# Kernel tuning notes

Hardware: AMD Instinct MI355X
Metric: run time of the kernel (lower is better)

The kernel has to match this reference:

```python
import jax, jax.numpy as jnp
import numpy as np

B, T, D = 2, 2048, 2048
H, HKV, HD = 32, 8, 64
THETA = 3.0
EPS = 1e-6
SCALE = HD ** -0.5


def _rms(x, w):
    # x: [..., HD]
    return x * jax.lax.rsqrt(jnp.mean(x * x, axis=-1, keepdims=True) + EPS) * w


def _rope(x):
    # x: [B, h, T, HD]; interleaved-pair rotation, matching RotaryEmbedding
    hd = x.shape[-1]
    inv_freq = 1.0 / (THETA ** (jnp.arange(0, hd, 2, dtype=jnp.float32) / hd))  # [hd/2]
    t = jnp.arange(x.shape[-2], dtype=jnp.float32)
    f = t[:, None] * inv_freq[None, :]  # [T, hd/2]
    c, s = jnp.cos(f), jnp.sin(f)
    x1, x2 = x[..., 0::2], x[..., 1::2]
    return jnp.stack([x1 * c - x2 * s, x1 * s + x2 * c], axis=-1).reshape(x.shape)


def setup_inputs() -> dict:
    key = jax.random.key(0)
    ks = jax.random.split(key, 6)
    x = jax.random.normal(ks[0], (B, T, D), dtype=jnp.float32)
    w_scale = 1.0 / np.sqrt(D)
    Wq = jax.random.normal(ks[1], (H * HD, D), dtype=jnp.float32) * w_scale
    Wk = jax.random.normal(ks[2], (HKV * HD, D), dtype=jnp.float32) * w_scale
    Wv = jax.random.normal(ks[3], (HKV * HD, D), dtype=jnp.float32) * w_scale
    Wo = jax.random.normal(ks[4], (D, H * HD), dtype=jnp.float32) * (1.0 / np.sqrt(H * HD))
    q_norm_w = jnp.ones((HD,), dtype=jnp.float32)
    k_norm_w = jnp.ones((HD,), dtype=jnp.float32)
    causal = jnp.tril(jnp.ones((T, T), dtype=bool))
    mask = jnp.where(causal, 0.0, -1e9).astype(jnp.float32)[None, None]  # [1,1,T,T]
    return dict(x=x, Wq=Wq, Wk=Wk, Wv=Wv, Wo=Wo, q_norm_w=q_norm_w, k_norm_w=k_norm_w, mask=mask)


def reference(x, Wq, Wk, Wv, Wo, q_norm_w, k_norm_w, mask):
    b, t, _ = x.shape
    q = (x @ Wq.T).reshape(b, t, H, HD).transpose(0, 2, 1, 3)      # [B,H,T,HD]
    k = (x @ Wk.T).reshape(b, t, HKV, HD).transpose(0, 2, 1, 3)    # [B,HKV,T,HD]
    v = (x @ Wv.T).reshape(b, t, HKV, HD).transpose(0, 2, 1, 3)
    q = _rms(q, q_norm_w)
    k = _rms(k, k_norm_w)
    q = _rope(q)
    k = _rope(k)
    rep = H // HKV
    k = jnp.repeat(k, rep, axis=1)  # GQA expansion -> [B,H,T,HD]
    v = jnp.repeat(v, rep, axis=1)
    scores = jnp.einsum('bhqd,bhkd->bhqk', q, k) * SCALE + mask
    attn = jax.nn.softmax(scores, axis=-1)
    out = jnp.einsum('bhqk,bhkd->bhqd', attn, v)
    out = out.transpose(0, 2, 1, 3).reshape(b, t, H * HD)
    return out @ Wo.T
```

## Files before the change

kernel.cpp:

```cpp
#include <hip/hip_runtime.h>
#include <hip/hip_bf16.h>
#include <stdint.h>

#define B_ 2
#define T_ 2048
#define D_ 2048
#define H_ 32
#define HKV_ 8
#define HD_ 64
#define SCALE_ 0.125f

typedef float floatx4 __attribute__((ext_vector_type(4)));
typedef __bf16 bf16x8 __attribute__((ext_vector_type(8)));
typedef __bf16 bf16x4 __attribute__((ext_vector_type(4)));
typedef short short4v __attribute__((ext_vector_type(4)));

__device__ inline floatx4 mfma16(bf16x8 a, bf16x8 b, floatx4 c) {
  return __builtin_amdgcn_mfma_f32_16x16x32_bf16(a, b, c, 0, 0, 0);
}

__device__ inline floatx4 mfma16k16(bf16x4 a, bf16x4 b, floatx4 c) {
#if __has_builtin(__builtin_amdgcn_mfma_f32_16x16x16_bf16)
  return __builtin_amdgcn_mfma_f32_16x16x16_bf16(a, b, c, 0, 0, 0);
#else
  return __builtin_amdgcn_mfma_f32_16x16x16bf16_1k(
      __builtin_bit_cast(short4v, a), __builtin_bit_cast(short4v, b), c, 0, 0, 0);
#endif
}

__device__ inline uint16_t f2bf(float f) {
  union { float f; uint32_t u; } x; x.f = f;
  uint32_t r = x.u + 0x7fffu + ((x.u >> 16) & 1u);
  return (uint16_t)(r >> 16);
}

__device__ inline uint32_t f2bf_pk(float a, float b) {
#if __has_builtin(__builtin_amdgcn_cvt_pk_bf16_f32)
  auto pk = __builtin_amdgcn_cvt_pk_bf16_f32(a, b);
  return __builtin_bit_cast(uint32_t, pk);
#else
  return (uint32_t)f2bf(a) | ((uint32_t)f2bf(b) << 16);
#endif
}

__device__ inline uint32_t pack_p(float a, float b) {
#if __has_builtin(__builtin_amdgcn_cvt_pk_bf16_f32)
  auto pk = __builtin_amdgcn_cvt_pk_bf16_f32(a, b);
  return __builtin_bit_cast(uint32_t, pk);
#else
  return __builtin_amdgcn_perm(__builtin_bit_cast(uint32_t, b),
                               __builtin_bit_cast(uint32_t, a), 0x07060302u);
#endif
}

__device__ inline float fast_exp2(float x) {
#if __has_builtin(__builtin_amdgcn_exp2f)
  return __builtin_amdgcn_exp2f(x);
#else
  return __expf(x * 0.69314718056f);
#endif
}

#if __has_builtin(__builtin_amdgcn_global_load_lds)
#define HAVE_ASYNC_LDS 1
typedef const __attribute__((address_space(1))) uint32_t* gas1_u32;
typedef __attribute__((address_space(3))) uint32_t* las3_u32;
__device__ inline void g2lds16(const uint16_t* g, uint16_t* l) {
  __builtin_amdgcn_global_load_lds((gas1_u32)(const void*)g, (las3_u32)(void*)l, 16, 0, 0);
}
#endif

__global__ __launch_bounds__(256) void cvt_all(
    const float* __restrict__ x, const float* __restrict__ wq,
    const float* __restrict__ wk, const float* __restrict__ wv,
    const float* __restrict__ wo,
    uint16_t* __restrict__ xb, uint16_t* __restrict__ wqb,
    uint16_t* __restrict__ wkb, uint16_t* __restrict__ wvb,
    uint16_t* __restrict__ wob) {
  int i = blockIdx.x * 256 + threadIdx.x;
  const float* src; uint16_t* dst; int off;
  if (i < 2097152)      { src = x;  dst = xb;  off = i; }
  else if (i < 3145728) { src = wq; dst = wqb; off = i - 2097152; }
  else if (i < 3407872) { src = wk; dst = wkb; off = i - 3145728; }
  else if (i < 3670016) { src = wv; dst = wvb; off = i - 3407872; }
  else                  { src = wo; dst = wob; off = i - 3670016; }
  float4 v = ((const float4*)src)[off];
  uint64_t packed = (uint64_t)f2bf_pk(v.x, v.y) | ((uint64_t)f2bf_pk(v.z, v.w) << 32);
  ((uint64_t*)dst)[off] = packed;
}

#define BM 128
#define BN 128

__device__ inline bf16x8 frag32(const uint16_t* lds, int row, int quad) {
  int pcg = quad ^ ((row >> 1) & 3);
  return *(const bf16x8*)&lds[row * 32 + pcg * 8];
}


#define GEMM_PROLOGUE()                                                    \
  const int srow = tid >> 2;                                               \
  const int scg = (tid & 3) ^ ((tid >> 3) & 3);                            \
  const uint16_t* gA0 = Abase + (size_t)srow * D_ + scg * 8;               \
  const uint16_t* gA1 = gA0 + (size_t)64 * D_;                             \
  const uint16_t* gB0 = Bbase + (size_t)srow * D_ + scg * 8;               \
  const uint16_t* gB1 = gB0 + (size_t)64 * D_;                             \
  uint16_t* lA[2] = {As + tid * 8, As + 4096 + tid * 8};                   \
  uint16_t* lB[2] = {Bs + tid * 8, Bs + 4096 + tid * 8};

#ifdef HAVE_ASYNC_LDS
#define GEMM_STAGE(buf, k)                                                 \
  { g2lds16(gA0 + (k), lA[buf]); g2lds16(gA1 + (k), lA[buf] + 2048);       \
    g2lds16(gB0 + (k), lB[buf]); g2lds16(gB1 + (k), lB[buf] + 2048); }
#else
#define GEMM_STAGE(buf, k)                                                 \
  { *(uint4*)lA[buf] = *(const uint4*)(gA0 + (k));                         \
    *(uint4*)(lA[buf] + 2048) = *(const uint4*)(gA1 + (k));                \
    *(uint4*)lB[buf] = *(const uint4*)(gB0 + (k));                         \
    *(uint4*)(lB[buf] + 2048) = *(const uint4*)(gB1 + (k)); }
#endif

#define GEMM_KLOOP()                                                       \
  GEMM_PROLOGUE()                                                          \
  GEMM_STAGE(0, 0)                                                         \
  int cur = 0;                                                             \
  for (int k0 = 0; k0 < D_; k0 += 32) {                                    \
    __syncthreads();                                                       \
    if (k0 + 32 < D_) { GEMM_STAGE(cur ^ 1, k0 + 32) }                     \
    const uint16_t* Ac = As + cur * 4096;                                  \
    const uint16_t* Bc = Bs + cur * 4096;                                  \
    bf16x8 af[4], bfr[4];                                                  \
    _Pragma("unroll")                                                      \
    for (int i = 0; i < 4; i++) af[i] = frag32(Ac, wm + i * 16 + r16, quad); \
    _Pragma("unroll")                                                      \
    for (int j = 0; j < 4; j++) bfr[j] = frag32(Bc, wn + j * 16 + r16, quad); \
    _Pragma("unroll")                                                      \
    for (int i = 0; i < 4; i++)                                            \
      _Pragma("unroll")                                                    \
      for (int j = 0; j < 4; j++)                                          \
        acc[i][j] = mfma16(af[i], bfr[j], acc[i][j]);                      \
    cur ^= 1;                                                              \
  }

__global__ __launch_bounds__(256) void qkv_gemm(
    const uint16_t* __restrict__ Xb, const uint16_t* __restrict__ Wqb,
    const uint16_t* __restrict__ Wkb, const uint16_t* __restrict__ Wvb,
    const float* __restrict__ qnw, const float* __restrict__ knw,
    uint16_t* __restrict__ qbf, uint16_t* __restrict__ kbf,
    uint16_t* __restrict__ vt) {
  __shared__ __align__(16) uint16_t As[2 * BM * 32];
  __shared__ __align__(16) uint16_t Bs[2 * BN * 32];
  const int tid = threadIdx.x;
  const int m0 = blockIdx.y * BM;
  const int n0 = blockIdx.x * BN;

  const uint16_t* Wsrc; int nbase;
  if (n0 < 2048)      { Wsrc = Wqb; nbase = 0; }
  else if (n0 < 2560) { Wsrc = Wkb; nbase = 2048; }
  else                { Wsrc = Wvb; nbase = 2560; }

  const int lane = tid & 63, wave = tid >> 6;
  const int wm = (wave >> 1) * 64, wn = (wave & 1) * 64;
  const int quad = lane >> 4, r16 = lane & 15;
  const uint16_t* Abase = Xb + (size_t)m0 * D_;
  const uint16_t* Bbase = Wsrc + (size_t)(n0 - nbase) * D_;

  floatx4 acc[4][4];
  #pragma unroll
  for (int i = 0; i < 4; i++)
    #pragma unroll
    for (int j = 0; j < 4; j++) acc[i][j] = (floatx4){0.f, 0.f, 0.f, 0.f};

  GEMM_KLOOP()

  if (n0 < 2560) {
    const int isK = (n0 >= 2048);
    const float* nw = isK ? knw : qnw;
    const int head = (n0 - (isK ? 2048 : 0) + wn) >> 6;
    uint16_t* dst = isK ? kbf : qbf;
    const int NH = isK ? HKV_ : H_;
    float wreg[4];
    #pragma unroll
    for (int j = 0; j < 4; j++) wreg[j] = nw[j * 16 + r16];
    float freq[4];
    #pragma unroll
    for (int j = 0; j < 4; j++)
      freq[j] = exp2f((float)(j * 8 + (r16 >> 1)) * -0.0495300781f);
    #pragma unroll
    for (int i = 0; i < 4; i++) {
      #pragma unroll
      for (int r = 0; r < 4; r++) {
        float ss = 0.f;
        #pragma unroll
        for (int j = 0; j < 4; j++) ss += acc[i][j][r] * acc[i][j][r];
        #pragma unroll
        for (int off = 8; off; off >>= 1) ss += __shfl_xor(ss, off);
        float inv = rsqrtf(ss * (1.0f / HD_) + 1e-6f);
        int m = m0 + wm + i * 16 + quad * 4 + r;
        int b = m >> 11, t = m & (T_ - 1);
        size_t rowbase = (((size_t)b * NH + head) * T_ + t) * HD_;
        #pragma unroll
        for (int j = 0; j < 4; j++) {
          float vn = acc[i][j][r] * inv * wreg[j];
          float other = __shfl_xor(vn, 1);
          float f = (float)t * freq[j];
          float s, c;
          __sincosf(f, &s, &c);
          float outv = (r16 & 1) ? (other * s + vn * c) : (vn * c - other * s);
          dst[rowbase + j * 16 + r16] = f2bf(outv);
        }
      }
    }
  } else {
    #pragma unroll
    for (int i = 0; i < 4; i++)
      #pragma unroll
      for (int j = 0; j < 4; j++)
        #pragma unroll
        for (int r = 0; r < 4; r++) {
          int m = m0 + wm + i * 16 + quad * 4 + r;
          int n = n0 + wn + j * 16 + r16 - 2560;
          int b = m >> 11, t = m & (T_ - 1);
          int head = n >> 6, d = n & 63;
          vt[(((size_t)b * HKV_ + head) * HD_ + d) * T_ + t] = f2bf(acc[i][j][r]);
        }
  }
}

__global__ __launch_bounds__(256) void oproj_gemm(
    const uint16_t* __restrict__ Ab, const uint16_t* __restrict__ Bb,
    float* __restrict__ C) {
  __shared__ __align__(16) uint16_t As[2 * BM * 32];
  __shared__ __align__(16) uint16_t Bs[2 * BN * 32];
  const int tid = threadIdx.x;
  const int m0 = blockIdx.y * BM;
  const int n0 = blockIdx.x * BN;
  const int lane = tid & 63, wave = tid >> 6;
  const int wm = (wave >> 1) * 64, wn = (wave & 1) * 64;
  const int quad = lane >> 4, r16 = lane & 15;
  const uint16_t* Abase = Ab + (size_t)m0 * D_;
  const uint16_t* Bbase = Bb + (size_t)n0 * D_;

  floatx4 acc[4][4];
  #pragma unroll
  for (int i = 0; i < 4; i++)
    #pragma unroll
    for (int j = 0; j < 4; j++) acc[i][j] = (floatx4){0.f, 0.f, 0.f, 0.f};

  GEMM_KLOOP()

  #pragma unroll
  for (int i = 0; i < 4; i++)
    #pragma unroll
    for (int j = 0; j < 4; j++)
      #pragma unroll
      for (int r = 0; r < 4; r++) {
        int m = m0 + wm + i * 16 + quad * 4 + r;
        int n = n0 + wn + j * 16 + r16;
        C[(size_t)m * D_ + n] = acc[i][j][r];
      }
}

#define LOG2E 1.44269504089f

__global__ __launch_bounds__(256) void attn(const uint16_t* __restrict__ qb,
                                            const uint16_t* __restrict__ kb,
                                            const uint16_t* __restrict__ vtb,
                                            uint16_t* __restrict__ ao) {
  const int tid = threadIdx.x;
  const int wave = tid >> 6, lane = tid & 63;
  const int quad = lane >> 4, r16 = lane & 15;
  const int h = blockIdx.y, b = blockIdx.z;
  const int kvh = h >> 2;

  const uint16_t* Q  = qb  + ((size_t)b * H_ + h) * T_ * HD_;
  const uint16_t* K  = kb  + ((size_t)b * HKV_ + kvh) * T_ * HD_;
  const uint16_t* Vt = vtb + ((size_t)b * HKV_ + kvh) * (size_t)HD_ * T_;

  __shared__ __align__(16) uint16_t Kl[2][64 * 64];
  __shared__ __align__(16) uint16_t Vl[2][64 * 64];

  const int l3 = lane >> 3, l7 = lane & 7, l4 = lane >> 4;
  const int cgK  = l7 ^ l3;
  const int cgV0 = l7 ^ (l4 & 7);
  const int cgV1 = l7 ^ ((4 + l4) & 7);
  const int sOff = wave * 16 * 64 + lane * 8;

  const int koffE0 = r16 * 64 + ((quad)     ^ (r16 & 7)) * 8;
  const int koffE1 = r16 * 64 + ((4 + quad) ^ (r16 & 7)) * 8;
  int voffE[4];
  #pragma unroll
  for (int mt = 0; mt < 4; mt++)
    voffE[mt] = r16 * 64 + (((mt * 2 + (quad >> 1)) ^ ((r16 >> 1) & 7)) * 8) + (quad & 1) * 4;
  float dm[4];
  #pragma unroll
  for (int r = 0; r < 4; r++) dm[r] = (quad * 4 + r <= r16) ? 1.0f : 0.0f;

#ifdef HAVE_ASYNC_LDS
#define AT_STAGE(buf)                                                     \
  { g2lds16(kg0, &Kl[buf][sOff]); g2lds16(kg1, &Kl[buf][sOff + 512]);     \
    g2lds16(vg0, &Vl[buf][sOff]); g2lds16(vg1, &Vl[buf][sOff + 512]);     \
    kg0 += 64 * HD_; kg1 += 64 * HD_; vg0 += 64; vg1 += 64; }
#else
#define AT_STAGE(buf)                                                     \
  { *(uint4*)&Kl[buf][sOff] = *(const uint4*)kg0;                         \
    *(uint4*)&Kl[buf][sOff + 512] = *(const uint4*)kg1;                   \
    *(uint4*)&Vl[buf][sOff] = *(const uint4*)vg0;                         \
    *(uint4*)&Vl[buf][sOff + 512] = *(const uint4*)vg1;                   \
    kg0 += 64 * HD_; kg1 += 64 * HD_; vg0 += 64; vg1 += 64; }
#endif

#define AT_CHUNK(mt, MASKED)                                              \
  {                                                                       \
    bf16x8 kf0 = *(const bf16x8*)&Kc[koffE0 + (mt) * 1024];               \
    bf16x8 kf1 = *(const bf16x8*)&Kc[koffE1 + (mt) * 1024];               \
    floatx4 st = (floatx4){0.f, 0.f, 0.f, 0.f};                           \
    st = mfma16(kf0, bq[0], st);                                          \
    st = mfma16(kf1, bq[1], st);                                          \
    float pv[4];                                                          \
    _Pragma("unroll")                                                     \
    for (int r = 0; r < 4; r++) {                                         \
      pv[r] = fast_exp2(fmaf(st[r], SCALE_ * LOG2E, -8.0f * LOG2E));      \
      if (MASKED) pv[r] *= dm[r];                                         \
      l += pv[r];                                                         \
    }                                                                     \
    uint64_t pu = (uint64_t)pack_p(pv[0], pv[1]) |                        \
                  ((uint64_t)pack_p(pv[2], pv[3]) << 32);                 \
    bf16x4 pa = __builtin_bit_cast(bf16x4, pu);                           \
    _Pragma("unroll")                                                     \
    for (int jn = 0; jn < 4; jn++) {                                      \
      bf16x4 vf = *(const bf16x4*)&Vc[voffE[mt] + jn * 1024];             \
      o[jn] = mfma16k16(pa, vf, o[jn]);                                   \
    }                                                                     \
  }

  for (int pass = 0; pass < 2; pass++) {
    const int qt = pass ? (int)blockIdx.x : 31 - (int)blockIdx.x;
    const int q0 = qt * 64;
    const int Rw = q0 + wave * 16;

    bf16x8 bq[2];
    #pragma unroll
    for (int hh = 0; hh < 2; hh++)
      bq[hh] = *(const bf16x8*)(Q + (size_t)(Rw + r16) * HD_ + hh * 32 + quad * 8);

    floatx4 o[4];
    float l = 0.f;
    #pragma unroll
    for (int jn = 0; jn < 4; jn++) o[jn] = (floatx4){0.f, 0.f, 0.f, 0.f};

    const uint16_t* kg0 = K + (size_t)(wave * 16 + l3) * HD_ + cgK * 8;
    const uint16_t* kg1 = K + (size_t)(wave * 16 + 8 + l3) * HD_ + cgK * 8;
    const uint16_t* vg0 = Vt + (size_t)(wave * 16 + l3) * T_ + cgV0 * 8;
    const uint16_t* vg1 = Vt + (size_t)(wave * 16 + 8 + l3) * T_ + cgV1 * 8;

    __syncthreads();
    AT_STAGE(0)
    int cur = 0;

    for (int it = 0; it < qt; it++) {
      __syncthreads();
      AT_STAGE(cur ^ 1)
      const uint16_t* Kc = Kl[cur];
      const uint16_t* Vc = Vl[cur];
      AT_CHUNK(0, false)
      AT_CHUNK(1, false)
      AT_CHUNK(2, false)
      AT_CHUNK(3, false)
      cur ^= 1;
    }
    __syncthreads();
    {
      const uint16_t* Kc = Kl[cur];
      const uint16_t* Vc = Vl[cur];
      #pragma unroll
      for (int mt = 0; mt < 4; mt++) {
        if (mt < wave) AT_CHUNK(mt, false)
        else if (mt == wave) AT_CHUNK(mt, true)
      }
    }

    l += __shfl_xor(l, 16);
    l += __shfl_xor(l, 32);
    float lq[4];
    #pragma unroll
    for (int r = 0; r < 4; r++) lq[r] = __shfl(l, quad * 4 + r);

    #pragma unroll
    for (int jn = 0; jn < 4; jn++) {
      uint32_t u01 = f2bf_pk(o[jn][0] / lq[0], o[jn][1] / lq[1]);
      uint32_t u23 = f2bf_pk(o[jn][2] / lq[2], o[jn][3] / lq[3]);
      int t0 = Rw + quad * 4;
      size_t base = ((size_t)b * T_ + t0) * (H_ * HD_) + h * HD_ + jn * 16 + r16;
      ao[base]                = (uint16_t)u01;
      ao[base + 1 * H_ * HD_] = (uint16_t)(u01 >> 16);
      ao[base + 2 * H_ * HD_] = (uint16_t)u23;
      ao[base + 3 * H_ * HD_] = (uint16_t)(u23 >> 16);
    }
  }
#undef AT_STAGE
#undef AT_CHUNK
}

extern "C" void kernel_launch(void* const* d_in, const int* in_sizes, int n_in,
                              void* d_out, int out_size, void* d_ws, size_t ws_size,
                              hipStream_t stream) {
  const float* x  = (const float*)d_in[0];
  const float* Wq = (const float*)d_in[1];
  const float* Wk = (const float*)d_in[2];
  const float* Wv = (const float*)d_in[3];
  const float* Wo = (const float*)d_in[4];
  const float* qw = (const float*)d_in[5];
  const float* kw = (const float*)d_in[6];
  float* out = (float*)d_out;

  char* ws = (char*)d_ws;
  uint16_t* xb  = (uint16_t*)(ws);
  uint16_t* wqb = (uint16_t*)(ws + 16777216);
  uint16_t* wkb = (uint16_t*)(ws + 25165824);
  uint16_t* wvb = (uint16_t*)(ws + 27262976);
  uint16_t* wob = (uint16_t*)(ws + 29360128);
  uint16_t* qbf = (uint16_t*)(ws + 37748736);
  uint16_t* kbf = (uint16_t*)(ws + 54525952);
  uint16_t* vtb = (uint16_t*)(ws + 58720256);
  uint16_t* aob = xb;

  cvt_all<<<18432, 256, 0, stream>>>(x, Wq, Wk, Wv, Wo, xb, wqb, wkb, wvb, wob);

  qkv_gemm<<<dim3(24, 32), 256, 0, stream>>>(xb, wqb, wkb, wvb, qw, kw, qbf, kbf, vtb);

  attn<<<dim3(16, 32, 2), 256, 0, stream>>>(qbf, kbf, vtb, aob);

  oproj_gemm<<<dim3(16, 32), 256, 0, stream>>>(aob, wob, out);
}
```

Measured before the change: 314.0 us.

## Rewrite QKV and output GEMMs with 256x256 tiles, 8 waves, explicit pipelining

```diff
diff --git a/kernel.cpp b/kernel.cpp
--- a/kernel.cpp
+++ b/kernel.cpp
@@ -89,175 +89,190 @@
   ((uint64_t*)dst)[off] = packed;
 }
 
-#define BM 128
-#define BN 128
-
-__device__ inline bf16x8 frag32(const uint16_t* lds, int row, int quad) {
-  int pcg = quad ^ ((row >> 1) & 3);
-  return *(const bf16x8*)&lds[row * 32 + pcg * 8];
-}
-
-
-#define GEMM_PROLOGUE()                                                    \
-  const int srow = tid >> 2;                                               \
-  const int scg = (tid & 3) ^ ((tid >> 3) & 3);                            \
-  const uint16_t* gA0 = Abase + (size_t)srow * D_ + scg * 8;               \
-  const uint16_t* gA1 = gA0 + (size_t)64 * D_;                             \
-  const uint16_t* gB0 = Bbase + (size_t)srow * D_ + scg * 8;               \
-  const uint16_t* gB1 = gB0 + (size_t)64 * D_;                             \
-  uint16_t* lA[2] = {As + tid * 8, As + 4096 + tid * 8};                   \
-  uint16_t* lB[2] = {Bs + tid * 8, Bs + 4096 + tid * 8};
+#define NT2 32
 
 #ifdef HAVE_ASYNC_LDS
-#define GEMM_STAGE(buf, k)                                                 \
-  { g2lds16(gA0 + (k), lA[buf]); g2lds16(gA1 + (k), lA[buf] + 2048);       \
-    g2lds16(gB0 + (k), lB[buf]); g2lds16(gB1 + (k), lB[buf] + 2048); }
-#else
-#define GEMM_STAGE(buf, k)                                                 \
-  { *(uint4*)lA[buf] = *(const uint4*)(gA0 + (k));                         \
-    *(uint4*)(lA[buf] + 2048) = *(const uint4*)(gA1 + (k));                \
-    *(uint4*)lB[buf] = *(const uint4*)(gB0 + (k));                         \
-    *(uint4*)(lB[buf] + 2048) = *(const uint4*)(gB1 + (k)); }
-#endif
-
-#define GEMM_KLOOP()                                                       \
-  GEMM_PROLOGUE()                                                          \
-  GEMM_STAGE(0, 0)                                                         \
-  int cur = 0;                                                             \
-  for (int k0 = 0; k0 < D_; k0 += 32) {                                    \
-    __syncthreads();                                                       \
-    if (k0 + 32 < D_) { GEMM_STAGE(cur ^ 1, k0 + 32) }                     \
-    const uint16_t* Ac = As + cur * 4096;                                  \
-    const uint16_t* Bc = Bs + cur * 4096;                                  \
-    bf16x8 af[4], bfr[4];                                                  \
-    _Pragma("unroll")                                                      \
-    for (int i = 0; i < 4; i++) af[i] = frag32(Ac, wm + i * 16 + r16, quad); \
-    _Pragma("unroll")                                                      \
-    for (int j = 0; j < 4; j++) bfr[j] = frag32(Bc, wn + j * 16 + r16, quad); \
-    _Pragma("unroll")                                                      \
-    for (int i = 0; i < 4; i++)                                            \
-      _Pragma("unroll")                                                    \
-      for (int j = 0; j < 4; j++)                                          \
-        acc[i][j] = mfma16(af[i], bfr[j], acc[i][j]);                      \
-    cur ^= 1;                                                              \
+#define ST_A(buf, band, koff) \
+  g2lds16(gA + (size_t)(band) * (64 * D_) + (koff), &As[buf][(band) * 4096 + tid * 8]);
+#define ST_B(buf, band, koff) \
+  g2lds16(gB + (size_t)(band) * (64 * D_) + (koff), &Bs[buf][(band) * 4096 + tid * 8]);
+#else
+#define ST_A(buf, band, koff) \
+  *(uint4*)&As[buf][(band) * 4096 + tid * 8] = \
+      *(const uint4*)(gA + (size_t)(band) * (64 * D_) + (koff));
+#define ST_B(buf, band, koff) \
+  *(uint4*)&Bs[buf][(band) * 4096 + tid * 8] = \
+      *(const uint4*)(gB + (size_t)(band) * (64 * D_) + (koff));
+#endif
+
+#define LDS_A4(bc, mib, kh)                                                  \
+  _Pragma("unroll")                                                          \
+  for (int mi_ = 0; mi_ < 4; mi_++)                                          \
+    aF[mi_] = *(const bf16x8*)&As[bc][aBase + ((mib) + mi_) * 1024 + ((kh) ? o1 : o0)];
+#define LDS_B4(bc, kh)                                                       \
+  _Pragma("unroll")                                                          \
+  for (int ni_ = 0; ni_ < 4; ni_++)                                          \
+    bF[ni_] = *(const bf16x8*)&Bs[bc][bBase + ni_ * 1024 + ((kh) ? o1 : o0)];
+
+#define MFMA_PH(MB)                                                          \
+  asm volatile("s_barrier\n\ts_waitcnt lgkmcnt(0)" ::: "memory");            \
+  __builtin_amdgcn_s_setprio(1);                                             \
+  _Pragma("unroll")                                                          \
+  for (int mi_ = 0; mi_ < 4; mi_++)                                          \
+    _Pragma("unroll")                                                        \
+    for (int ni_ = 0; ni_ < 4; ni_++)                                        \
+      acc[(MB) + mi_][ni_] = mfma16(aF[mi_], bF[ni_], acc[(MB) + mi_][ni_]); \
+  __builtin_amdgcn_s_setprio(0);                                             \
+  asm volatile("s_barrier" ::: "memory");
+
+#define TILE(bc, P0S, P0T, P3S, P3T, VMS)                                    \
+  {                                                                          \
+    asm volatile("s_waitcnt vmcnt(" VMS ")\n\ts_barrier" ::: "memory");      \
+    LDS_A4(bc, 0, 0) LDS_B4(bc, 0)                                           \
+    if (P0S) { ST_A((bc) ^ 1, 1, (P0T) * 64) ST_A((bc) ^ 1, 3, (P0T) * 64) } \
+    MFMA_PH(0)                                                               \
+    LDS_A4(bc, 4, 0)                                                         \
+    MFMA_PH(4)                                                               \
+    LDS_A4(bc, 0, 1) LDS_B4(bc, 1)                                           \
+    MFMA_PH(0)                                                               \
+    LDS_A4(bc, 4, 1)                                                         \
+    if (P3S) { ST_A(bc, 0, (P3T) * 64) ST_A(bc, 2, (P3T) * 64)               \
+               ST_B(bc, 0, (P3T) * 64) ST_B(bc, 1, (P3T) * 64)               \
+               ST_B(bc, 2, (P3T) * 64) ST_B(bc, 3, (P3T) * 64) }             \
+    MFMA_PH(4)                                                               \
   }
 
-__global__ __launch_bounds__(256) void qkv_gemm(
+#define G8_SETUP()                                                           \
+  const int tid = threadIdx.x;                                               \
+  const int lane = tid & 63, wave = tid >> 6;                                \
+  const int w_m = wave >> 2, w_n = wave & 3;                                 \
+  const int quad = lane >> 4, r16 = lane & 15;                               \
+  const int pa_ = quad ^ (r16 & 7);                                          \
+  const int o0 = pa_ * 8, o1 = (pa_ ^ 4) * 8;                                \
+  const int aBase = (w_m * 128 + r16) * 64;                                  \
+  const int bBase = (w_n * 64 + r16) * 64;                                   \
+  const int srow = tid >> 3;                                                 \
+  const uint16_t* gA = Abase + (size_t)srow * D_ + ((tid & 7) ^ (srow & 7)) * 8; \
+  const uint16_t* gB = Bbase + (size_t)srow * D_ + ((tid & 7) ^ (srow & 7)) * 8; \
+  bf16x8 aF[4], bF[4];                                                       \
+  floatx4 acc[8][4];                                                         \
+  _Pragma("unroll")                                                          \
+  for (int i_ = 0; i_ < 8; i_++)                                             \
+    _Pragma("unroll")                                                        \
+    for (int j_ = 0; j_ < 4; j_++) acc[i_][j_] = (floatx4){0.f, 0.f, 0.f, 0.f};
+
+#define G8_KLOOP()                                                           \
+  ST_A(0, 0, 0) ST_A(0, 2, 0) ST_B(0, 0, 0)                                  \
+  ST_B(0, 1, 0) ST_B(0, 2, 0) ST_B(0, 3, 0)                                  \
+  asm volatile("" ::: "memory");                                             \
+  ST_A(0, 1, 0) ST_A(0, 3, 0)                                                \
+  asm volatile("" ::: "memory");                                             \
+  ST_A(1, 0, 64) ST_A(1, 2, 64) ST_B(1, 0, 64)                               \
+  ST_B(1, 1, 64) ST_B(1, 2, 64) ST_B(1, 3, 64)                               \
+  for (int j = 0; j < NT2 - 2; j += 2) {                                     \
+    TILE(0, 1, j + 1, 1, j + 2, "6")                                         \
+    TILE(1, 1, j + 2, 1, j + 3, "6")                                         \
+  }                                                                          \
+  TILE(0, 1, NT2 - 1, 0, 0, "6")                                             \
+  TILE(1, 0, 0, 0, 0, "0")
+
+__global__ __launch_bounds__(512, 2) void qkv_gemm(
     const uint16_t* __restrict__ Xb, const uint16_t* __restrict__ Wqb,
     const uint16_t* __restrict__ Wkb, const uint16_t* __restrict__ Wvb,
     const float* __restrict__ qnw, const float* __restrict__ knw,
     uint16_t* __restrict__ qbf, uint16_t* __restrict__ kbf,
     uint16_t* __restrict__ vt) {
-  __shared__ __align__(16) uint16_t As[2 * BM * 32];
-  __shared__ __align__(16) uint16_t Bs[2 * BN * 32];
-  const int tid = threadIdx.x;
-  const int m0 = blockIdx.y * BM;
-  const int n0 = blockIdx.x * BN;
+  __shared__ __align__(16) uint16_t As[2][16384];
+  __shared__ __align__(16) uint16_t Bs[2][16384];
+  const int m0 = blockIdx.y * 256;
+  const int n0 = blockIdx.x * 256;
 
   const uint16_t* Wsrc; int nbase;
   if (n0 < 2048)      { Wsrc = Wqb; nbase = 0; }
   else if (n0 < 2560) { Wsrc = Wkb; nbase = 2048; }
   else                { Wsrc = Wvb; nbase = 2560; }
 
-  const int lane = tid & 63, wave = tid >> 6;
-  const int wm = (wave >> 1) * 64, wn = (wave & 1) * 64;
-  const int quad = lane >> 4, r16 = lane & 15;
   const uint16_t* Abase = Xb + (size_t)m0 * D_;
   const uint16_t* Bbase = Wsrc + (size_t)(n0 - nbase) * D_;
 
-  floatx4 acc[4][4];
-  #pragma unroll
-  for (int i = 0; i < 4; i++)
-    #pragma unroll
-    for (int j = 0; j < 4; j++) acc[i][j] = (floatx4){0.f, 0.f, 0.f, 0.f};
-
-  GEMM_KLOOP()
+  G8_SETUP()
+  G8_KLOOP()
 
   if (n0 < 2560) {
     const int isK = (n0 >= 2048);
     const float* nw = isK ? knw : qnw;
-    const int head = (n0 - (isK ? 2048 : 0) + wn) >> 6;
+    const int head = ((n0 - (isK ? 2048 : 0)) >> 6) + w_n;
     uint16_t* dst = isK ? kbf : qbf;
     const int NH = isK ? HKV_ : H_;
-    float wreg[4];
-    #pragma unroll
-    for (int j = 0; j < 4; j++) wreg[j] = nw[j * 16 + r16];
-    float freq[4];
-    #pragma unroll
-    for (int j = 0; j < 4; j++)
-      freq[j] = exp2f((float)(j * 8 + (r16 >> 1)) * -0.0495300781f);
-    #pragma unroll
-    for (int i = 0; i < 4; i++) {
+    float wreg[4], freq[4];
+    #pragma unroll
+    for (int ni = 0; ni < 4; ni++) {
+      wreg[ni] = nw[ni * 16 + r16];
+      freq[ni] = exp2f((float)(ni * 8 + (r16 >> 1)) * -0.0495300781f);
+    }
+    #pragma unroll
+    for (int mi = 0; mi < 8; mi++) {
       #pragma unroll
       for (int r = 0; r < 4; r++) {
         float ss = 0.f;
         #pragma unroll
-        for (int j = 0; j < 4; j++) ss += acc[i][j][r] * acc[i][j][r];
+        for (int ni = 0; ni < 4; ni++) ss += acc[mi][ni][r] * acc[mi][ni][r];
         #pragma unroll
         for (int off = 8; off; off >>= 1) ss += __shfl_xor(ss, off);
         float inv = rsqrtf(ss * (1.0f / HD_) + 1e-6f);
-        int m = m0 + wm + i * 16 + quad * 4 + r;
-        int b = m >> 11, t = m & (T_ - 1);
-        size_t rowbase = (((size_t)b * NH + head) * T_ + t) * HD_;
+        int m = m0 + w_m * 128 + mi * 16 + quad * 4 + r;
+        int bb = m >> 11, tt = m & (T_ - 1);
+        size_t rowbase = (((size_t)bb * NH + head) * T_ + tt) * HD_;
         #pragma unroll
-        for (int j = 0; j < 4; j++) {
-          float vn = acc[i][j][r] * inv * wreg[j];
+        for (int ni = 0; ni < 4; ni++) {
+          float vn = acc[mi][ni][r] * inv * wreg[ni];
           float other = __shfl_xor(vn, 1);
-          float f = (float)t * freq[j];
+          float f = (float)tt * freq[ni];
           float s, c;
           __sincosf(f, &s, &c);
           float outv = (r16 & 1) ? (other * s + vn * c) : (vn * c - other * s);
-          dst[rowbase + j * 16 + r16] = f2bf(outv);
+          dst[rowbase + ni * 16 + r16] = f2bf(outv);
         }
       }
     }
   } else {
     #pragma unroll
-    for (int i = 0; i < 4; i++)
+    for (int mi = 0; mi < 8; mi++)
       #pragma unroll
-      for (int j = 0; j < 4; j++)
+      for (int ni = 0; ni < 4; ni++)
         #pragma unroll
         for (int r = 0; r < 4; r++) {
-          int m = m0 + wm + i * 16 + quad * 4 + r;
-          int n = n0 + wn + j * 16 + r16 - 2560;
-          int b = m >> 11, t = m & (T_ - 1);
-          int head = n >> 6, d = n & 63;
-          vt[(((size_t)b * HKV_ + head) * HD_ + d) * T_ + t] = f2bf(acc[i][j][r]);
+          int m = m0 + w_m * 128 + mi * 16 + quad * 4 + r;
+          int n = n0 + w_n * 64 + ni * 16 + r16 - 2560;
+          int bb = m >> 11, tt = m & (T_ - 1);
+          vt[(((size_t)bb * HKV_ + (n >> 6)) * HD_ + (n & 63)) * T_ + tt] =
+              f2bf(acc[mi][ni][r]);
         }
   }
 }
 
-__global__ __launch_bounds__(256) void oproj_gemm(
+__global__ __launch_bounds__(512, 2) void oproj_gemm(
     const uint16_t* __restrict__ Ab, const uint16_t* __restrict__ Bb,
     float* __restrict__ C) {
-  __shared__ __align__(16) uint16_t As[2 * BM * 32];
-  __shared__ __align__(16) uint16_t Bs[2 * BN * 32];
-  const int tid = threadIdx.x;
-  const int m0 = blockIdx.y * BM;
-  const int n0 = blockIdx.x * BN;
-  const int lane = tid & 63, wave = tid >> 6;
-  const int wm = (wave >> 1) * 64, wn = (wave & 1) * 64;
-  const int quad = lane >> 4, r16 = lane & 15;
+  __shared__ __align__(16) uint16_t As[2][16384];
+  __shared__ __align__(16) uint16_t Bs[2][16384];
+  const int m0 = blockIdx.y * 256;
+  const int n0 = blockIdx.x * 256;
   const uint16_t* Abase = Ab + (size_t)m0 * D_;
   const uint16_t* Bbase = Bb + (size_t)n0 * D_;
 
-  floatx4 acc[4][4];
+  G8_SETUP()
+  G8_KLOOP()
+
   #pragma unroll
-  for (int i = 0; i < 4; i++)
-    #pragma unroll
-    for (int j = 0; j < 4; j++) acc[i][j] = (floatx4){0.f, 0.f, 0.f, 0.f};
-
-  GEMM_KLOOP()
-
-  #pragma unroll
-  for (int i = 0; i < 4; i++)
-    #pragma unroll
-    for (int j = 0; j < 4; j++)
+  for (int mi = 0; mi < 8; mi++)
+    #pragma unroll
+    for (int ni = 0; ni < 4; ni++)
       #pragma unroll
       for (int r = 0; r < 4; r++) {
-        int m = m0 + wm + i * 16 + quad * 4 + r;
-        int n = n0 + wn + j * 16 + r16;
-        C[(size_t)m * D_ + n] = acc[i][j][r];
+        int m = m0 + w_m * 128 + mi * 16 + quad * 4 + r;
+        int n = n0 + w_n * 64 + ni * 16 + r16;
+        C[(size_t)m * D_ + n] = acc[mi][ni][r];
       }
 }
 
@@ -427,9 +442,9 @@
 
   cvt_all<<<18432, 256, 0, stream>>>(x, Wq, Wk, Wv, Wo, xb, wqb, wkb, wvb, wob);
 
-  qkv_gemm<<<dim3(24, 32), 256, 0, stream>>>(xb, wqb, wkb, wvb, qw, kw, qbf, kbf, vtb);
+  qkv_gemm<<<dim3(12, 16), 512, 0, stream>>>(xb, wqb, wkb, wvb, qw, kw, qbf, kbf, vtb);
 
   attn<<<dim3(16, 32, 2), 256, 0, stream>>>(qbf, kbf, vtb, aob);
 
-  oproj_gemm<<<dim3(16, 32), 256, 0, stream>>>(aob, wob, out);
-}
+  oproj_gemm<<<dim3(8, 16), 512, 0, stream>>>(aob, wob, out);
+}
```

Result: no change. 314.0 us (-0.0%).

## Remap block indices for XCD-aware L2 locality and raise MFMA wave priority

Applied to the files above, without the earlier changes.

```diff
diff --git a/kernel.cpp b/kernel.cpp
--- a/kernel.cpp
+++ b/kernel.cpp
@@ -151,8 +151,10 @@
   __shared__ __align__(16) uint16_t As[2 * BM * 32];
   __shared__ __align__(16) uint16_t Bs[2 * BN * 32];
   const int tid = threadIdx.x;
-  const int m0 = blockIdx.y * BM;
-  const int n0 = blockIdx.x * BN;
+  const int lin = (int)blockIdx.y * 24 + (int)blockIdx.x;
+  const int s = (lin & 7) * 96 + (lin >> 3);
+  const int m0 = (s / 24) * BM;
+  const int n0 = (s % 24) * BN;
 
   const uint16_t* Wsrc; int nbase;
   if (n0 < 2048)      { Wsrc = Wqb; nbase = 0; }
@@ -204,9 +206,9 @@
           float vn = acc[i][j][r] * inv * wreg[j];
           float other = __shfl_xor(vn, 1);
           float f = (float)t * freq[j];
-          float s, c;
-          __sincosf(f, &s, &c);
-          float outv = (r16 & 1) ? (other * s + vn * c) : (vn * c - other * s);
+          float s2, c2;
+          __sincosf(f, &s2, &c2);
+          float outv = (r16 & 1) ? (other * s2 + vn * c2) : (vn * c2 - other * s2);
           dst[rowbase + j * 16 + r16] = f2bf(outv);
         }
       }
@@ -233,8 +235,10 @@
   __shared__ __align__(16) uint16_t As[2 * BM * 32];
   __shared__ __align__(16) uint16_t Bs[2 * BN * 32];
   const int tid = threadIdx.x;
-  const int m0 = blockIdx.y * BM;
-  const int n0 = blockIdx.x * BN;
+  const int lin = (int)blockIdx.y * 16 + (int)blockIdx.x;
+  const int s = (lin & 7) * 64 + (lin >> 3);
+  const int m0 = (s >> 4) * BM;
+  const int n0 = (s & 15) * BN;
   const int lane = tid & 63, wave = tid >> 6;
   const int wm = (wave >> 1) * 64, wn = (wave & 1) * 64;
   const int quad = lane >> 4, r16 = lane & 15;
@@ -270,7 +274,11 @@
   const int tid = threadIdx.x;
   const int wave = tid >> 6, lane = tid & 63;
   const int quad = lane >> 4, r16 = lane & 15;
-  const int h = blockIdx.y, b = blockIdx.z;
+  const int lin = ((int)blockIdx.z * 32 + (int)blockIdx.y) * 16 + (int)blockIdx.x;
+  const int s = (lin & 7) * 128 + (lin >> 3);
+  const int bx = s & 15;
+  const int h  = (s >> 4) & 31;
+  const int b  = s >> 9;
   const int kvh = h >> 2;
 
   const uint16_t* Q  = qb  + ((size_t)b * H_ + h) * T_ * HD_;
@@ -315,8 +323,10 @@
     bf16x8 kf0 = *(const bf16x8*)&Kc[koffE0 + (mt) * 1024];               \
     bf16x8 kf1 = *(const bf16x8*)&Kc[koffE1 + (mt) * 1024];               \
     floatx4 st = (floatx4){0.f, 0.f, 0.f, 0.f};                           \
+    __builtin_amdgcn_s_setprio(1);                                        \
     st = mfma16(kf0, bq[0], st);                                          \
     st = mfma16(kf1, bq[1], st);                                          \
+    __builtin_amdgcn_s_setprio(0);                                        \
     float pv[4];                                                          \
     _Pragma("unroll")                                                     \
     for (int r = 0; r < 4; r++) {                                         \
@@ -327,15 +337,17 @@
     uint64_t pu = (uint64_t)pack_p(pv[0], pv[1]) |                        \
                   ((uint64_t)pack_p(pv[2], pv[3]) << 32);                 \
     bf16x4 pa = __builtin_bit_cast(bf16x4, pu);                           \
+    __builtin_amdgcn_s_setprio(1);                                        \
     _Pragma("unroll")                                                     \
     for (int jn = 0; jn < 4; jn++) {                                      \
       bf16x4 vf = *(const bf16x4*)&Vc[voffE[mt] + jn * 1024];             \
       o[jn] = mfma16k16(pa, vf, o[jn]);                                   \
     }                                                                     \
+    __builtin_amdgcn_s_setprio(0);                                        \
   }
 
   for (int pass = 0; pass < 2; pass++) {
-    const int qt = pass ? (int)blockIdx.x : 31 - (int)blockIdx.x;
+    const int qt = pass ? bx : 31 - bx;
     const int q0 = qt * 64;
     const int Rw = q0 + wave * 16;
 
```

New measurement: 313.1 us. About the same (-0.3%).
